# Kernel tuning notes

Hardware: AMD Instinct MI355X
Metric: run time of the kernel (lower is better)

Reference implementation:

```python
import jax, jax.numpy as jnp
import numpy as np

B, N, C, H = 8, 1024, 1024, 16
D = C // H
DFF = 4 * C
EPS = 1e-6


def _ln(x):
    mu = jnp.mean(x, axis=-1, keepdims=True)
    var = jnp.mean(jnp.square(x - mu), axis=-1, keepdims=True)
    return (x - mu) / jnp.sqrt(var + EPS)


def _modulate(x, shift, scale):
    return x * (1 + scale) + shift


def setup_inputs() -> dict:
    key = jax.random.key(0)
    ks = jax.random.split(key, 12)
    s = 0.02
    inp = {
        "x": jax.random.normal(ks[0], (B, N, C), jnp.float32),
        "c": jax.random.normal(ks[1], (B, 1, C), jnp.float32),
        "causal_mask": jnp.tril(jnp.ones((N, N), jnp.int32))[None, None],  # [1,1,N,N]
        "qkv_w": jax.random.normal(ks[2], (3 * C, C), jnp.float32) * s,
        "qkv_b": jnp.zeros((3 * C,), jnp.float32),
        "proj_w": jax.random.normal(ks[3], (C, C), jnp.float32) * s,
        "proj_b": jnp.zeros((C,), jnp.float32),
        "fc1_w": jax.random.normal(ks[4], (DFF, C), jnp.float32) * s,
        "fc1_b": jnp.zeros((DFF,), jnp.float32),
        "fc2_w": jax.random.normal(ks[5], (C, DFF), jnp.float32) * s,
        "fc2_b": jnp.zeros((C,), jnp.float32),
        "ada_w": jax.random.normal(ks[6], (6 * C, C), jnp.float32) * s,
        "ada_b": jnp.zeros((6 * C,), jnp.float32),
    }
    return inp


def reference(x, c, causal_mask, qkv_w, qkv_b, proj_w, proj_b,
              fc1_w, fc1_b, fc2_w, fc2_b, ada_w, ada_b):
    # adaLN modulation: SiLU -> Linear(C -> 6C) -> chunk 6
    mod = jax.nn.silu(c) @ ada_w.T + ada_b  # [B,1,6C]
    (shift_msa, scale_msa, gate_msa,
     shift_mlp, scale_mlp, gate_mlp) = jnp.split(mod, 6, axis=-1)

    # --- causal attention ---
    y = _modulate(_ln(x), shift_msa, scale_msa)  # [B,N,C]
    qkv = y @ qkv_w.T + qkv_b                    # [B,N,3C]
    qkv = qkv.reshape(B, N, 3, H, D).transpose(2, 0, 3, 1, 4)  # [3,B,H,N,D]
    q, k, v = qkv[0], qkv[1], qkv[2]
    scale = D ** -0.5
    attn = jnp.einsum('bhnd,bhmd->bhnm', q, k) * scale  # [B,H,N,N]
    attn = jnp.where(causal_mask == 0, -jnp.inf, attn)
    attn = jax.nn.softmax(attn, axis=-1)
    o = jnp.einsum('bhnm,bhmd->bhnd', attn, v)
    o = o.transpose(0, 2, 1, 3).reshape(B, N, C)
    o = o @ proj_w.T + proj_b
    x = x + gate_msa * o

    # --- MLP ---
    z = _modulate(_ln(x), shift_mlp, scale_mlp)
    h = jax.nn.gelu(z @ fc1_w.T + fc1_b, approximate=True)
    m = h @ fc2_w.T + fc2_b
    x = x + gate_mlp * m
    return x
```

## Files before the change

kernel.cpp:

```cpp
#include <hip/hip_runtime.h>
#include <math.h>
#include <stdint.h>
#include <stddef.h>

namespace {

constexpr int kB = 8, kN = 1024, kC = 1024, kH = 16, kD = 64, kDFF = 4096;
constexpr int kM = kB * kN;
constexpr int k6C = 6 * kC;
constexpr float kQKScale = 0.18033688011112042f;
constexpr float kM8 = 8.0f;

typedef _Float16 half8 __attribute__((ext_vector_type(8)));
typedef _Float16 half4v __attribute__((ext_vector_type(4)));
typedef float f32x4 __attribute__((ext_vector_type(4)));
typedef int v4i __attribute__((ext_vector_type(4)));
typedef signed char i8;

__device__ inline void ld_lds16(const void* g, void* l) {
  __builtin_amdgcn_global_load_lds(
      (const __attribute__((address_space(1))) void*)g,
      (__attribute__((address_space(3))) void*)l, 16, 0, 0);
}

__device__ inline int xcd_swizzle(int flat, int nwg) {
  return (flat & 7) * (nwg >> 3) + (flat >> 3);
}

__device__ inline unsigned pack4_i8(float y0, float y1, float y2, float y3, float inv) {
  int q0 = (int)rintf(y0 * inv), q1 = (int)rintf(y1 * inv);
  int q2 = (int)rintf(y2 * inv), q3 = (int)rintf(y3 * inv);
  q0 = min(max(q0, -127), 127); q1 = min(max(q1, -127), 127);
  q2 = min(max(q2, -127), 127); q3 = min(max(q3, -127), 127);
  return (unsigned)(q0 & 0xFF) | ((unsigned)(q1 & 0xFF) << 8) |
         ((unsigned)(q2 & 0xFF) << 16) | ((unsigned)(q3 & 0xFF) << 24);
}

__global__ void cvt_f32_f16(const float* __restrict__ src, _Float16* __restrict__ dst) {
  size_t i = (size_t)blockIdx.x * 256 + threadIdx.x;
  float4 f = ((const float4*)src)[i];
  half4v h;
  h[0] = (_Float16)f.x; h[1] = (_Float16)f.y; h[2] = (_Float16)f.z; h[3] = (_Float16)f.w;
  ((half4v*)dst)[i] = h;
}

__global__ __launch_bounds__(256) void quant_w_kernel(
    const float* __restrict__ src, i8* __restrict__ dst, float* __restrict__ wscale) {
  int n = blockIdx.x, tid = threadIdx.x;
  const float* row = src + (size_t)n * kC;
  float4 f = ((const float4*)row)[tid];
  float m = fmaxf(fmaxf(fabsf(f.x), fabsf(f.y)), fmaxf(fabsf(f.z), fabsf(f.w)));
#pragma unroll
  for (int msk = 32; msk; msk >>= 1) m = fmaxf(m, __shfl_xor(m, msk));
  __shared__ float red[4];
  int w = tid >> 6, lane = tid & 63;
  if (lane == 0) red[w] = m;
  __syncthreads();
  m = fmaxf(fmaxf(red[0], red[1]), fmaxf(red[2], red[3]));
  m = fmaxf(m, 1e-12f);
  float inv = 127.f / m;
  ((unsigned*)(dst + (size_t)n * kC))[tid] = pack4_i8(f.x, f.y, f.z, f.w, inv);
  if (tid == 0) wscale[n] = m * (1.f / 127.f);
}

__global__ __launch_bounds__(256) void mod_kernel(
    const float* __restrict__ c, const float* __restrict__ ada_w,
    const float* __restrict__ ada_b, float* __restrict__ mod) {
  __shared__ float sc[kC];
  int b  = blockIdx.x / (k6C / 4);
  int j0 = (blockIdx.x % (k6C / 4)) * 4;
  int tid = threadIdx.x;
  for (int i = tid; i < kC; i += 256) {
    float v = c[b * kC + i];
    sc[i] = v / (1.f + expf(-v));
  }
  __syncthreads();
  int w = tid >> 6, lane = tid & 63;
  int j = j0 + w;
  const float* wr = ada_w + (size_t)j * kC;
  float acc = 0.f;
#pragma unroll
  for (int kk = 0; kk < kC / 64; ++kk) {
    int k = kk * 64 + lane;
    acc += sc[k] * wr[k];
  }
#pragma unroll
  for (int m = 32; m; m >>= 1) acc += __shfl_xor(acc, m);
  if (lane == 0) mod[b * k6C + j] = acc + ada_b[j];
}

template <typename T>
__global__ __launch_bounds__(256) void ln_mod_q_kernel(
    const T* __restrict__ x, const float* __restrict__ mod,
    i8* __restrict__ out, float* __restrict__ ascale,
    int shift_off, int scale_off) {
  int row = blockIdx.x;
  int b = row >> 10;
  const T* xr = x + (size_t)row * kC;
  int tid = threadIdx.x;
  int cc0 = tid * 4;
  float v[4];
  float s = 0.f, s2 = 0.f;
#pragma unroll
  for (int i = 0; i < 4; ++i) {
    v[i] = (float)xr[cc0 + i];
    s += v[i];
    s2 += v[i] * v[i];
  }
#pragma unroll
  for (int m = 32; m; m >>= 1) { s += __shfl_xor(s, m); s2 += __shfl_xor(s2, m); }
  __shared__ float red[8];
  __shared__ float redm[4];
  int w = tid >> 6, lane = tid & 63;
  if (lane == 0) { red[w] = s; red[4 + w] = s2; }
  __syncthreads();
  s  = red[0] + red[1] + red[2] + red[3];
  s2 = red[4] + red[5] + red[6] + red[7];
  float mu   = s * (1.f / kC);
  float var  = s2 * (1.f / kC) - mu * mu;
  float rstd = rsqrtf(var + 1e-6f);
  const float* mb = mod + (size_t)b * k6C;
  float y[4];
  float m = 0.f;
#pragma unroll
  for (int i = 0; i < 4; ++i) {
    y[i] = (v[i] - mu) * rstd * (1.f + mb[scale_off + cc0 + i]) + mb[shift_off + cc0 + i];
    m = fmaxf(m, fabsf(y[i]));
  }
#pragma unroll
  for (int msk = 32; msk; msk >>= 1) m = fmaxf(m, __shfl_xor(m, msk));
  if (lane == 0) redm[w] = m;
  __syncthreads();
  m = fmaxf(fmaxf(redm[0], redm[1]), fmaxf(redm[2], redm[3]));
  m = fmaxf(m, 1e-12f);
  float inv = 127.f / m;
  ((unsigned*)(out + (size_t)row * kC))[tid] = pack4_i8(y[0], y[1], y[2], y[3], inv);
  if (tid == 0) ascale[row] = m * (1.f / 127.f);
}

template <int EPI>
__global__ __launch_bounds__(256) void gemm_i8_kernel(
    const i8* __restrict__ A, const i8* __restrict__ W,
    const float* __restrict__ ascale, const float* __restrict__ wscale,
    const float* __restrict__ bias, _Float16* __restrict__ outp,
    int M, int Nn, int K) {
  __shared__ __align__(16) i8 S[2 * 128 * 128];
  i8* As = S;
  i8* Bs = S + 128 * 128;
  int tid = threadIdx.x;
  int nwg = (int)(gridDim.x * gridDim.y);
  int swz = xcd_swizzle((int)(blockIdx.y * gridDim.x + blockIdx.x), nwg);
  int bn = swz % (int)gridDim.x, bm = swz / (int)gridDim.x;
  int lane = tid & 63, w = tid >> 6;
  int l15 = lane & 15, quad = lane >> 4;
  int wr = (w >> 1) * 64, wc = (w & 1) * 64;

  v4i acc[4][4];
#pragma unroll
  for (int i = 0; i < 4; ++i)
#pragma unroll
    for (int j = 0; j < 4; ++j) acc[i][j] = (v4i){0, 0, 0, 0};

  const i8* Ag = A + (size_t)bm * 128 * K;
  const i8* Wg = W + (size_t)bn * 128 * K;
  int r8 = lane >> 3;
  int jcb = ((lane & 7) ^ r8) * 16;

  for (int kt = 0; kt < K; kt += 128) {
#pragma unroll
    for (int u = 0; u < 4; ++u) {
      int row = w * 32 + u * 8 + r8;
      ld_lds16(&Ag[(size_t)row * K + kt + jcb], &As[(w * 32 + u * 8) * 128]);
      ld_lds16(&Wg[(size_t)row * K + kt + jcb], &Bs[(w * 32 + u * 8) * 128]);
    }
    __syncthreads();
    int sxor = l15 & 7;
    int c0 = (quad ^ sxor) * 16;
    int c1 = ((4 + quad) ^ sxor) * 16;
    v4i af[4][2], bf[4][2];
#pragma unroll
    for (int i = 0; i < 4; ++i) {
      const i8* rp = &As[(wr + i * 16 + l15) * 128];
      af[i][0] = *(const v4i*)&rp[c0];
      af[i][1] = *(const v4i*)&rp[c1];
    }
#pragma unroll
    for (int j = 0; j < 4; ++j) {
      const i8* rp = &Bs[(wc + j * 16 + l15) * 128];
      bf[j][0] = *(const v4i*)&rp[c0];
      bf[j][1] = *(const v4i*)&rp[c1];
    }
#pragma unroll
    for (int i = 0; i < 4; ++i)
#pragma unroll
      for (int j = 0; j < 4; ++j) {
        acc[i][j] = __builtin_amdgcn_mfma_i32_16x16x64_i8(af[i][0], bf[j][0], acc[i][j], 0, 0, 0);
        acc[i][j] = __builtin_amdgcn_mfma_i32_16x16x64_i8(af[i][1], bf[j][1], acc[i][j], 0, 0, 0);
      }
    __syncthreads();
  }

  _Float16* Cs = (_Float16*)S;
  int row0 = wr + quad * 4;
  int col0 = wc + l15;
#pragma unroll
  for (int i = 0; i < 4; ++i) {
#pragma unroll
    for (int j = 0; j < 4; ++j) {
      int colL = col0 + j * 16;
      int n = bn * 128 + colL;
      float ws = wscale[n];
      float bv = bias[n];
#pragma unroll
      for (int r = 0; r < 4; ++r) {
        int rowL = row0 + i * 16 + r;
        float as = ascale[bm * 128 + rowL];
        float v = (float)acc[i][j][r] * (as * ws) + bv;
        if constexpr (EPI == 0) {
          if (n < kC) v *= kQKScale;
        } else {
          float u = v + 0.044715f * v * v * v;
          v = v / (1.f + exp2f(-2.302208f * u));
        }
        Cs[rowL * 128 + (((colL >> 3) ^ (rowL & 7)) << 3) + (colL & 7)] = (_Float16)v;
      }
    }
  }
  __syncthreads();
#pragma unroll
  for (int p = 0; p < 8; ++p) {
    int r = (tid >> 4) + p * 16;
    int cc = tid & 15;
    half8 hv = *(const half8*)&Cs[r * 128 + ((cc ^ (r & 7)) << 3)];
    size_t gm = (size_t)(bm * 128 + r);
    int coff = bn * 128 + cc * 8;
    *(half8*)&outp[gm * Nn + coff] = hv;
  }
}

template <int EPI>
__global__ __launch_bounds__(256) void gemm_f16_kernel(
    const _Float16* __restrict__ A, const _Float16* __restrict__ W,
    const float* __restrict__ bias, void* __restrict__ outp,
    const void* __restrict__ resid, const float* __restrict__ mod,
    int M, int Nn, int K, int gate_off) {
  __shared__ __align__(16) _Float16 S[2 * 2 * 128 * 64];
  int tid = threadIdx.x;
  int nwg = (int)(gridDim.x * gridDim.y);
  int swz = xcd_swizzle((int)(blockIdx.y * gridDim.x + blockIdx.x), nwg);
  int bn = swz % (int)gridDim.x, bm = swz / (int)gridDim.x;
  int lane = tid & 63, w = tid >> 6;
  int l15 = lane & 15, quad = lane >> 4;
  int wr = (w >> 1) * 64, wc = (w & 1) * 64;

  f32x4 acc[4][4];
#pragma unroll
  for (int i = 0; i < 4; ++i)
#pragma unroll
    for (int j = 0; j < 4; ++j) acc[i][j] = (f32x4){0.f, 0.f, 0.f, 0.f};

  const _Float16* Ag = A + (size_t)bm * 128 * K;
  const _Float16* Wg = W + (size_t)bn * 128 * K;
  int r8 = lane >> 3;
  int jc = ((lane & 7) ^ r8) * 8;

  int nk = K / 64;
  {
    _Float16* Asp = S;
    _Float16* Bsp = S + 128 * 64;
#pragma unroll
    for (int u = 0; u < 4; ++u) {
      int row = w * 32 + u * 8 + r8;
      ld_lds16(&Ag[(size_t)row * K + jc], &Asp[(w * 32 + u * 8) * 64]);
      ld_lds16(&Wg[(size_t)row * K + jc], &Bsp[(w * 32 + u * 8) * 64]);
    }
  }
  __syncthreads();

  for (int t = 0; t < nk; ++t) {
    const _Float16* As = S + (t & 1) * (2 * 128 * 64);
    const _Float16* Bs = As + 128 * 64;
    if (t + 1 < nk) {
      _Float16* Asn = S + ((t + 1) & 1) * (2 * 128 * 64);
      _Float16* Bsn = Asn + 128 * 64;
      int kt = (t + 1) * 64;
#pragma unroll
      for (int u = 0; u < 4; ++u) {
        int row = w * 32 + u * 8 + r8;
        ld_lds16(&Ag[(size_t)row * K + kt + jc], &Asn[(w * 32 + u * 8) * 64]);
        ld_lds16(&Wg[(size_t)row * K + kt + jc], &Bsn[(w * 32 + u * 8) * 64]);
      }
    }
#pragma unroll
    for (int kk = 0; kk < 2; ++kk) {
      half8 af[4], bf[4];
#pragma unroll
      for (int i = 0; i < 4; ++i)
        af[i] = *(const half8*)&As[(wr + i * 16 + l15) * 64 +
                                   (((kk * 4 + quad) ^ (l15 & 7)) * 8)];
#pragma unroll
      for (int j = 0; j < 4; ++j)
        bf[j] = *(const half8*)&Bs[(wc + j * 16 + l15) * 64 +
                                   (((kk * 4 + quad) ^ (l15 & 7)) * 8)];
#pragma unroll
      for (int i = 0; i < 4; ++i)
#pragma unroll
        for (int j = 0; j < 4; ++j)
          acc[i][j] = __builtin_amdgcn_mfma_f32_16x16x32_f16(af[i], bf[j], acc[i][j], 0, 0, 0);
    }
    __syncthreads();
  }

  _Float16* Cs = S;
  int row0 = wr + quad * 4;
  int col0 = wc + l15;
#pragma unroll
  for (int i = 0; i < 4; ++i) {
#pragma unroll
    for (int j = 0; j < 4; ++j) {
      int colL = col0 + j * 16;
      int n = bn * 128 + colL;
      float bv = bias[n];
#pragma unroll
      for (int r = 0; r < 4; ++r) {
        int rowL = row0 + i * 16 + r;
        float v = acc[i][j][r] + bv;
        Cs[rowL * 128 + (((colL >> 3) ^ (rowL & 7)) << 3) + (colL & 7)] = (_Float16)v;
      }
    }
  }
  __syncthreads();
  int b6 = (bm >> 3) * k6C + gate_off + bn * 128;
#pragma unroll
  for (int p = 0; p < 8; ++p) {
    int r = (tid >> 4) + p * 16;
    int cc = tid & 15;
    half8 hv = *(const half8*)&Cs[r * 128 + ((cc ^ (r & 7)) << 3)];
    size_t gm = (size_t)(bm * 128 + r);
    int coff = bn * 128 + cc * 8;
    if constexpr (EPI == 2) {
      const float* rp = &((const float*)resid)[gm * kC + coff];
      const float* gp = &mod[b6 + cc * 8];
      half8 ov;
#pragma unroll
      for (int e = 0; e < 8; ++e) ov[e] = (_Float16)(rp[e] + gp[e] * (float)hv[e]);
      *(half8*)&((_Float16*)outp)[gm * kC + coff] = ov;
    } else {
      const _Float16* rp = &((const _Float16*)resid)[gm * kC + coff];
      const float* gp = &mod[b6 + cc * 8];
      half8 rv = *(const half8*)rp;
      float ov[8];
#pragma unroll
      for (int e = 0; e < 8; ++e) ov[e] = (float)rv[e] + gp[e] * (float)hv[e];
      *(float4*)&((float*)outp)[gm * kC + coff] = *(float4*)&ov[0];
      *(float4*)&((float*)outp)[gm * kC + coff + 4] = *(float4*)&ov[4];
    }
  }
}

__global__ __launch_bounds__(256) void vtrans_kernel(
    const _Float16* __restrict__ qkv, _Float16* __restrict__ vT) {
  int nt = blockIdx.x, h = blockIdx.y, b = blockIdx.z;
  __shared__ _Float16 Ts[64 * 72];
  int tid = threadIdx.x;
  const _Float16* src = qkv + ((size_t)(b * kN + nt * 64)) * (3 * kC) + 2 * kC + h * 64;
#pragma unroll
  for (int u = 0; u < 2; ++u) {
    int idx = tid + u * 256;
    int r = idx >> 3, c8 = (idx & 7) * 8;
    *(uint4*)&Ts[r * 72 + c8] = *(const uint4*)&src[(size_t)r * (3 * kC) + c8];
  }
  __syncthreads();
  _Float16* dst = vT + (((size_t)(b * kH + h)) * 64) * kN + nt * 64;
#pragma unroll
  for (int u = 0; u < 2; ++u) {
    int idx = tid + u * 256;
    int d = idx >> 3, n8 = (idx & 7) * 8;
    half8 v;
#pragma unroll
    for (int e = 0; e < 8; ++e) v[e] = Ts[(n8 + e) * 72 + d];
    *(half8*)&dst[(size_t)d * kN + n8] = v;
  }
}

__global__ __launch_bounds__(256) void attn_kernel(
    const _Float16* __restrict__ qkv, const _Float16* __restrict__ vT,
    _Float16* __restrict__ o) {
  int nwg = (int)(gridDim.x * gridDim.y * gridDim.z);
  int flat = (int)((blockIdx.z * gridDim.y + blockIdx.y) * gridDim.x + blockIdx.x);
  int swz = xcd_swizzle(flat, nwg);
  int qt = swz % (int)gridDim.x;
  int tmp = swz / (int)gridDim.x;
  int h = tmp % (int)gridDim.y, b = tmp / (int)gridDim.y;
  __shared__ __align__(16) _Float16 Qs[128 * 64];
  __shared__ __align__(16) _Float16 Ks[64 * 64];
  __shared__ __align__(16) _Float16 Vs[64 * 64];
  __shared__ __align__(16) _Float16 Ps[128 * 72];
  int tid = threadIdx.x, lane = tid & 63, w = tid >> 6;
  int l15 = lane & 15, quad = lane >> 4;
  int wq = w * 32;
  int r8 = lane >> 3;
  int jc = ((lane & 7) ^ r8) * 8;

  const _Float16* Qg = qkv + ((size_t)(b * kN + qt * 128)) * (3 * kC) + h * kD;
  const _Float16* Kg = qkv + ((size_t)(b * kN)) * (3 * kC) + kC + h * kD;
  const _Float16* Vg = vT + ((size_t)(b * kH + h) * kD) * kN;

#pragma unroll
  for (int u = 0; u < 4; ++u)
    ld_lds16(&Qg[(size_t)(w * 32 + u * 8 + r8) * (3 * kC) + jc],
             &Qs[(w * 32 + u * 8) * 64]);
  __syncthreads();

  half8 aq[2][2];
#pragma unroll
  for (int i = 0; i < 2; ++i)
#pragma unroll
    for (int kk = 0; kk < 2; ++kk)
      aq[i][kk] = *(const half8*)&Qs[(wq + i * 16 + l15) * 64 +
                                     (((kk * 4 + quad) ^ (l15 & 7)) * 8)];

  f32x4 o_acc[2][4];
  f32x4 lsum[2];
#pragma unroll
  for (int i = 0; i < 2; ++i) {
    lsum[i] = (f32x4){0.f, 0.f, 0.f, 0.f};
#pragma unroll
    for (int dt = 0; dt < 4; ++dt) o_acc[i][dt] = (f32x4){0.f, 0.f, 0.f, 0.f};
  }
  half8 ones;
#pragma unroll
  for (int e = 0; e < 8; ++e) ones[e] = (_Float16)1.f;

  int jmax = 2 * qt + 2;
  for (int j = 0; j < jmax; ++j) {
#pragma unroll
    for (int u = 0; u < 2; ++u) {
      int row = w * 16 + u * 8 + r8;
      ld_lds16(&Kg[(size_t)(j * 64 + row) * (3 * kC) + jc], &Ks[(w * 16 + u * 8) * 64]);
      ld_lds16(&Vg[(size_t)row * kN + j * 64 + jc],         &Vs[(w * 16 + u * 8) * 64]);
    }
    __syncthreads();
    bool need_mask = (j >= 2 * qt);

    f32x4 s[2][4];
#pragma unroll
    for (int ct = 0; ct < 4; ++ct) {
      half8 b0 = *(const half8*)&Ks[(ct * 16 + l15) * 64 + ((quad ^ (l15 & 7)) * 8)];
      half8 b1 = *(const half8*)&Ks[(ct * 16 + l15) * 64 + (((4 + quad) ^ (l15 & 7)) * 8)];
#pragma unroll
      for (int i = 0; i < 2; ++i) {
        f32x4 t = (f32x4){0.f, 0.f, 0.f, 0.f};
        t = __builtin_amdgcn_mfma_f32_16x16x32_f16(aq[i][0], b0, t, 0, 0, 0);
        t = __builtin_amdgcn_mfma_f32_16x16x32_f16(aq[i][1], b1, t, 0, 0, 0);
        s[i][ct] = t;
      }
    }

#pragma unroll
    for (int i = 0; i < 2; ++i)
#pragma unroll
      for (int ct = 0; ct < 4; ++ct)
#pragma unroll
        for (int r = 0; r < 4; ++r) {
          float p = exp2f(fminf(s[i][ct][r] - kM8, 14.f));
          if (need_mask) {
            int kg = j * 64 + ct * 16 + l15;
            int qg = qt * 128 + wq + i * 16 + quad * 4 + r;
            if (kg > qg) p = 0.f;
          }
          Ps[(wq + i * 16 + quad * 4 + r) * 72 + ct * 16 + l15] = (_Float16)p;
        }

    half8 ap[2][2];
#pragma unroll
    for (int i = 0; i < 2; ++i) {
      ap[i][0] = *(const half8*)&Ps[(wq + i * 16 + l15) * 72 + quad * 8];
      ap[i][1] = *(const half8*)&Ps[(wq + i * 16 + l15) * 72 + 32 + quad * 8];
      lsum[i] = __builtin_amdgcn_mfma_f32_16x16x32_f16(ap[i][0], ones, lsum[i], 0, 0, 0);
      lsum[i] = __builtin_amdgcn_mfma_f32_16x16x32_f16(ap[i][1], ones, lsum[i], 0, 0, 0);
    }
#pragma unroll
    for (int dt = 0; dt < 4; ++dt) {
      half8 bv0 = *(const half8*)&Vs[(dt * 16 + l15) * 64 + ((quad ^ (l15 & 7)) * 8)];
      half8 bv1 = *(const half8*)&Vs[(dt * 16 + l15) * 64 + (((4 + quad) ^ (l15 & 7)) * 8)];
#pragma unroll
      for (int i = 0; i < 2; ++i) {
        o_acc[i][dt] = __builtin_amdgcn_mfma_f32_16x16x32_f16(ap[i][0], bv0, o_acc[i][dt], 0, 0, 0);
        o_acc[i][dt] = __builtin_amdgcn_mfma_f32_16x16x32_f16(ap[i][1], bv1, o_acc[i][dt], 0, 0, 0);
      }
    }
    __syncthreads();
  }

#pragma unroll
  for (int i = 0; i < 2; ++i) {
    float rl[4];
#pragma unroll
    for (int r = 0; r < 4; ++r) rl[r] = 1.f / lsum[i][r];
#pragma unroll
    for (int dt = 0; dt < 4; ++dt)
#pragma unroll
      for (int r = 0; r < 4; ++r) {
        int q = qt * 128 + wq + i * 16 + quad * 4 + r;
        o[((size_t)(b * kN + q)) * kC + h * kD + dt * 16 + l15] =
            (_Float16)(o_acc[i][dt][r] * rl[r]);
      }
  }
}

}

extern "C" void kernel_launch(void* const* d_in, const int* in_sizes, int n_in,
                              void* d_out, int out_size, void* d_ws, size_t ws_size,
                              hipStream_t stream) {
  const float* x      = (const float*)d_in[0];
  const float* c      = (const float*)d_in[1];
  const float* qkv_w  = (const float*)d_in[3];
  const float* qkv_b  = (const float*)d_in[4];
  const float* proj_w = (const float*)d_in[5];
  const float* proj_b = (const float*)d_in[6];
  const float* fc1_w  = (const float*)d_in[7];
  const float* fc1_b  = (const float*)d_in[8];
  const float* fc2_w  = (const float*)d_in[9];
  const float* fc2_b  = (const float*)d_in[10];
  const float* ada_w  = (const float*)d_in[11];
  const float* ada_b  = (const float*)d_in[12];
  float* out = (float*)d_out;

  char* ws = (char*)d_ws;
  float*    mod     = (float*)(ws);
  i8*       w_qkv   = (i8*)(ws + 196608);
  i8*       w_fc1   = (i8*)(ws + 3342336);
  _Float16* w_proj  = (_Float16*)(ws + 7536640);
  _Float16* w_fc2   = (_Float16*)(ws + 9633792);
  i8*       bufA    = (i8*)(ws + 18022400);
  float*    ascale  = (float*)(ws + 26411008);
  float*    ws_qkv  = (float*)(ws + 26443776);
  float*    ws_fc1  = (float*)(ws + 26456064);
  _Float16* vT      = (_Float16*)(ws + 26509312);
  _Float16* x2h     = (_Float16*)(ws + 26509312);
  _Float16* bufO    = (_Float16*)(ws + 43286528);
  _Float16* qkvh    = (_Float16*)(ws + 60063744);
  _Float16* hbuf    = (_Float16*)(ws + 60063744);

  quant_w_kernel<<<3 * kC, 256, 0, stream>>>(qkv_w, w_qkv, ws_qkv);
  quant_w_kernel<<<kDFF, 256, 0, stream>>>(fc1_w, w_fc1, ws_fc1);
  cvt_f32_f16<<<kC * kC / 1024, 256, 0, stream>>>(proj_w, w_proj);
  cvt_f32_f16<<<kC * kDFF / 1024, 256, 0, stream>>>(fc2_w, w_fc2);
  mod_kernel<<<kB * (k6C / 4), 256, 0, stream>>>(c, ada_w, ada_b, mod);
  ln_mod_q_kernel<float><<<kM, 256, 0, stream>>>(x, mod, bufA, ascale, 0, kC);
  gemm_i8_kernel<0><<<dim3(3 * kC / 128, kM / 128), 256, 0, stream>>>(
      bufA, w_qkv, ascale, ws_qkv, qkv_b, qkvh, kM, 3 * kC, kC);
  vtrans_kernel<<<dim3(kN / 64, kH, kB), 256, 0, stream>>>(qkvh, vT);
  attn_kernel<<<dim3(kN / 128, kH, kB), 256, 0, stream>>>(qkvh, vT, bufO);
  gemm_f16_kernel<2><<<dim3(kC / 128, kM / 128), 256, 0, stream>>>(
      bufO, w_proj, proj_b, x2h, x, mod, kM, kC, kC, 2 * kC);
  ln_mod_q_kernel<_Float16><<<kM, 256, 0, stream>>>(x2h, mod, bufA, ascale, 3 * kC, 4 * kC);
  gemm_i8_kernel<1><<<dim3(kDFF / 128, kM / 128), 256, 0, stream>>>(
      bufA, w_fc1, ascale, ws_fc1, fc1_b, hbuf, kM, kDFF, kC);
  gemm_f16_kernel<3><<<dim3(kC / 128, kM / 128), 256, 0, stream>>>(
      hbuf, w_fc2, fc2_b, out, x2h, mod, kM, kC, kDFF, 5 * kC);
}
```

Before: 478.1 us.

## Double-buffer int8 GEMM with 64-wide K tiles and use fast reciprocals

The int8 GEMM main loop now uses 64-wide K tiles held in two LDS buffers. The next tile's global-to-LDS loads are issued before the current tile's MFMAs, so only one barrier is needed per iteration and load latency overlaps with compute. LDS usage stays the same and a launch-bounds occupancy hint of 4 is added. Separately, the GELU epilogue and the attention normalisation replace full-precision division with the hardware reciprocal. This gives slightly lower precision, and the K step is halved, so there are twice as many loop iterations.

```diff
diff --git a/kernel.cpp b/kernel.cpp
--- a/kernel.cpp
+++ b/kernel.cpp
@@ -139,14 +139,12 @@
 }
 
 template <int EPI>
-__global__ __launch_bounds__(256) void gemm_i8_kernel(
+__global__ __launch_bounds__(256, 4) void gemm_i8_kernel(
     const i8* __restrict__ A, const i8* __restrict__ W,
     const float* __restrict__ ascale, const float* __restrict__ wscale,
     const float* __restrict__ bias, _Float16* __restrict__ outp,
     int M, int Nn, int K) {
-  __shared__ __align__(16) i8 S[2 * 128 * 128];
-  i8* As = S;
-  i8* Bs = S + 128 * 128;
+  __shared__ __align__(16) i8 S[2 * 2 * 128 * 64];
   int tid = threadIdx.x;
   int nwg = (int)(gridDim.x * gridDim.y);
   int swz = xcd_swizzle((int)(blockIdx.y * gridDim.x + blockIdx.x), nwg);
@@ -163,40 +161,51 @@
 
   const i8* Ag = A + (size_t)bm * 128 * K;
   const i8* Wg = W + (size_t)bn * 128 * K;
-  int r8 = lane >> 3;
-  int jcb = ((lane & 7) ^ r8) * 16;
-
-  for (int kt = 0; kt < K; kt += 128) {
-#pragma unroll
-    for (int u = 0; u < 4; ++u) {
-      int row = w * 32 + u * 8 + r8;
-      ld_lds16(&Ag[(size_t)row * K + kt + jcb], &As[(w * 32 + u * 8) * 128]);
-      ld_lds16(&Wg[(size_t)row * K + kt + jcb], &Bs[(w * 32 + u * 8) * 128]);
-    }
-    __syncthreads();
-    int sxor = l15 & 7;
-    int c0 = (quad ^ sxor) * 16;
-    int c1 = ((4 + quad) ^ sxor) * 16;
-    v4i af[4][2], bf[4][2];
-#pragma unroll
-    for (int i = 0; i < 4; ++i) {
-      const i8* rp = &As[(wr + i * 16 + l15) * 128];
-      af[i][0] = *(const v4i*)&rp[c0];
-      af[i][1] = *(const v4i*)&rp[c1];
-    }
-#pragma unroll
-    for (int j = 0; j < 4; ++j) {
-      const i8* rp = &Bs[(wc + j * 16 + l15) * 128];
-      bf[j][0] = *(const v4i*)&rp[c0];
-      bf[j][1] = *(const v4i*)&rp[c1];
-    }
+  int rg = lane >> 2;
+  int gsl = lane & 3;
+
+  int nk = K >> 6;
+  {
+    i8* As0 = S;
+    i8* Bs0 = S + 128 * 64;
+#pragma unroll
+    for (int s = 0; s < 2; ++s) {
+      int row = w * 32 + s * 16 + rg;
+      int gc = (gsl ^ ((row >> 1) & 3)) * 16;
+      ld_lds16(&Ag[(size_t)row * K + gc], &As0[(w * 32 + s * 16) * 64]);
+      ld_lds16(&Wg[(size_t)row * K + gc], &Bs0[(w * 32 + s * 16) * 64]);
+    }
+  }
+  __syncthreads();
+
+  int cread = (quad ^ ((l15 >> 1) & 3)) * 16;
+  for (int t = 0; t < nk; ++t) {
+    const i8* As = S + (t & 1) * (2 * 128 * 64);
+    const i8* Bs = As + 128 * 64;
+    if (t + 1 < nk) {
+      i8* Asn = S + ((t + 1) & 1) * (2 * 128 * 64);
+      i8* Bsn = Asn + 128 * 64;
+      int kt = (t + 1) << 6;
+#pragma unroll
+      for (int s = 0; s < 2; ++s) {
+        int row = w * 32 + s * 16 + rg;
+        int gc = (gsl ^ ((row >> 1) & 3)) * 16;
+        ld_lds16(&Ag[(size_t)row * K + kt + gc], &Asn[(w * 32 + s * 16) * 64]);
+        ld_lds16(&Wg[(size_t)row * K + kt + gc], &Bsn[(w * 32 + s * 16) * 64]);
+      }
+    }
+    v4i af[4], bf[4];
 #pragma unroll
     for (int i = 0; i < 4; ++i)
-#pragma unroll
-      for (int j = 0; j < 4; ++j) {
-        acc[i][j] = __builtin_amdgcn_mfma_i32_16x16x64_i8(af[i][0], bf[j][0], acc[i][j], 0, 0, 0);
-        acc[i][j] = __builtin_amdgcn_mfma_i32_16x16x64_i8(af[i][1], bf[j][1], acc[i][j], 0, 0, 0);
-      }
+      af[i] = *(const v4i*)&As[(wr + i * 16 + l15) * 64 + cread];
+#pragma unroll
+    for (int j = 0; j < 4; ++j)
+      bf[j] = *(const v4i*)&Bs[(wc + j * 16 + l15) * 64 + cread];
+#pragma unroll
+    for (int i = 0; i < 4; ++i)
+#pragma unroll
+      for (int j = 0; j < 4; ++j)
+        acc[i][j] = __builtin_amdgcn_mfma_i32_16x16x64_i8(af[i], bf[j], acc[i][j], 0, 0, 0);
     __syncthreads();
   }
 
@@ -220,7 +229,8 @@
           if (n < kC) v *= kQKScale;
         } else {
           float u = v + 0.044715f * v * v * v;
-          v = v / (1.f + exp2f(-2.302208f * u));
+          float t = exp2f(-2.302208f * u);
+          v = v * __builtin_amdgcn_rcpf(1.f + t);
         }
         Cs[rowL * 128 + (((colL >> 3) ^ (rowL & 7)) << 3) + (colL & 7)] = (_Float16)v;
       }
@@ -497,7 +507,7 @@
   for (int i = 0; i < 2; ++i) {
     float rl[4];
 #pragma unroll
-    for (int r = 0; r < 4; ++r) rl[r] = 1.f / lsum[i][r];
+    for (int r = 0; r < 4; ++r) rl[r] = __builtin_amdgcn_rcpf(lsum[i][r]);
 #pragma unroll
     for (int dt = 0; dt < 4; ++dt)
 #pragma unroll
```

Measured after the change: 465.2 us. -2.7%, faster.
